# Kernel tuning notes

Hardware: AMD Instinct MI355X
Metric: run time of the kernel (lower is better)

The kernel has to match this reference:

```python
import jax, jax.numpy as jnp
import numpy as np
from jax import lax

B, L, D_MODEL = 2, 4096, 1024
D_INNER = 2 * D_MODEL          # expand=2
D_STATE = D_INNER              # required: complex einsum contracts d_inner vs d_state
DT_RANK = 64                   # ceil(1024/16)
D_CONV = 4


def setup_inputs() -> dict:
    key = jax.random.key(0)
    ks = jax.random.split(key, 16)
    s = lambda *sh: 1.0 / np.sqrt(sh[-1])
    return {
        "hidden_states": jax.random.normal(ks[0], (B, L, D_MODEL), jnp.float32),
        "delta": jax.random.normal(ks[1], (B, L, DT_RANK), jnp.float32),
        # in_proj: Linear(d_model -> 2*d_inner), no bias
        "in_proj_w": jax.random.normal(ks[2], (2 * D_INNER, D_MODEL), jnp.float32) * s(D_MODEL),
        # depthwise causal conv1d: (out=d_inner, in/groups=1, k)
        "conv_w": jax.random.normal(ks[3], (D_INNER, 1, D_CONV), jnp.float32) * s(D_CONV),
        "conv_b": jax.random.normal(ks[4], (D_INNER,), jnp.float32) * 0.01,
        # ComplexStateSpace: only A_real affects the real output (x is real)
        "A_real": jax.random.normal(ks[5], (D_STATE, D_STATE), jnp.float32) * 0.1 / np.sqrt(D_STATE),
        # MIMO linears (torch Linear weight layout [out, in])
        "B_w": jax.random.normal(ks[6], (D_STATE, D_INNER), jnp.float32) * 0.1 * s(D_INNER),
        "C_w": jax.random.normal(ks[7], (D_INNER, D_STATE), jnp.float32) * 0.1 * s(D_STATE),
        "D_w": jax.random.normal(ks[8], (D_INNER, D_INNER), jnp.float32) * 0.1 * s(D_INNER),
        # SelectiveScan params
        "dt_proj_w": jax.random.normal(ks[9], (D_INNER, DT_RANK), jnp.float32) * 0.01,
        "dt_proj_b": jax.random.normal(ks[10], (D_INNER,), jnp.float32) * 0.01,
        "A_log": jax.random.uniform(ks[11], (D_INNER,), jnp.float32, -4.0, -1.0),
        "D_ss": jnp.ones((D_INNER,), jnp.float32),
        # out_proj: Linear(d_inner -> d_model), no bias
        "out_proj_w": jax.random.normal(ks[12], (D_MODEL, D_INNER), jnp.float32) * s(D_INNER),
    }


def reference(hidden_states, delta, in_proj_w, conv_w, conv_b, A_real,
              B_w, C_w, D_w, dt_proj_w, dt_proj_b, A_log, D_ss, out_proj_w):
    d_inner = A_log.shape[0]
    # in_proj + split
    xz = jnp.einsum('bld,ed->ble', hidden_states, in_proj_w)
    x, z = xz[..., :d_inner], xz[..., d_inner:]
    # depthwise causal conv1d (left-pad k-1 == torch pad both + truncate to L)
    xc = jnp.swapaxes(x, 1, 2)                      # [b, d, l]
    xc = lax.conv_general_dilated(xc, conv_w, window_strides=(1,),
                                  padding=[(D_CONV - 1, 0)],
                                  feature_group_count=d_inner)
    x = jnp.swapaxes(xc, 1, 2) + conv_b             # [b, l, d]
    x = jax.nn.silu(x)
    # ComplexStateSpace: real part of (x @ (A_real + iA_imag)) == x @ A_real
    x = x + jnp.einsum('bls,st->blt', x, A_real)
    # MIMO SSM: state_t = cumsum(B x)_t ; y_t = C state_t + D x_t  (vectorized)
    Bx = jnp.einsum('bld,sd->bls', x, B_w)          # [b, l, d_state]
    states = jnp.cumsum(Bx, axis=1)
    x_mimo = jnp.einsum('bls,es->ble', states, C_w) + jnp.einsum('bld,ed->ble', x, D_w)
    x = x + x_mimo
    # SelectiveScan: state = state * exp(dlt * A) + u, A = -exp(A_log)
    dlt = jax.nn.softplus(jnp.einsum('blr,dr->bld', delta, dt_proj_w) + dt_proj_b)
    decay = jnp.exp(dlt * (-jnp.exp(A_log)))        # [b, l, d], in (0, 1)

    def step(state, inp):
        dec, u = inp
        state = state * dec + u
        return state, state

    init = jnp.zeros_like(x[:, 0])
    _, scan_states = lax.scan(step, init,
                              (jnp.swapaxes(decay, 0, 1), jnp.swapaxes(x, 0, 1)))
    x = jnp.swapaxes(scan_states, 0, 1) + x * D_ss
    # gate + out projection
    out = x * jax.nn.silu(z)
    return jnp.einsum('ble,de->bld', out, out_proj_w)
```

## Files before the change

### kernel.cpp

```cpp
#include <hip/hip_runtime.h>
#include <cstdint>
#include <cstddef>


typedef unsigned short u16;
typedef __bf16 bf16x8 __attribute__((ext_vector_type(8)));
typedef float  f32x4  __attribute__((ext_vector_type(4)));

#define BDIM 256
#define M_ROWS 8192
#define LSEQ   4096
#define DI     2048
#define NCH    64
#define CLEN   64

__device__ __forceinline__ float bf2f(u16 h) {
    return __uint_as_float(((unsigned int)h) << 16);
}
__device__ __forceinline__ u16 f2bf(float f) {
    unsigned int u = __float_as_uint(f);
    u = u + 0x7fffu + ((u >> 16) & 1u);
    return (u16)(u >> 16);
}
__device__ __forceinline__ float siluf(float v) { return v / (1.0f + __expf(-v)); }

__device__ __forceinline__ void load16_to_lds(const u16* g, u16* l) {
    __builtin_amdgcn_global_load_lds((const __attribute__((address_space(1))) void*)g,
                                     (__attribute__((address_space(3))) void*)l,
                                     16, 0, 0);
}

__global__ void k_cvt_all(const float* __restrict__ hs, const float* __restrict__ inproj,
                          const float* __restrict__ Bw, const float* __restrict__ Cw,
                          const float* __restrict__ outw, const float* __restrict__ delta,
                          const float* __restrict__ dtw, const float* __restrict__ Areal,
                          const float* __restrict__ Dw, const float* __restrict__ Alog,
                          u16* __restrict__ XH, u16* __restrict__ W1, u16* __restrict__ WBb,
                          u16* __restrict__ WC, u16* __restrict__ WO, u16* __restrict__ DLT,
                          u16* __restrict__ WDT, u16* __restrict__ Pb, u16* __restrict__ Db,
                          float* __restrict__ NA) {
    long i = (long)(blockIdx.x * BDIM + threadIdx.x) * 4;
    if (i >= 32112640L) {
        long j = i - 32112640L;
        if (j < 2048) {
            float4 v = *reinterpret_cast<const float4*>(Alog + j);
            float4 o = {-__expf(v.x), -__expf(v.y), -__expf(v.z), -__expf(v.w)};
            *reinterpret_cast<float4*>(NA + j) = o;
        }
        return;
    }
    const float* src; u16* dst; long off; bool diag = false;
    if      (i <  8388608L) { src = hs;     dst = XH;  off = 0L; }
    else if (i < 12582912L) { src = inproj; dst = W1;  off = 8388608L; }
    else if (i < 16777216L) { src = Bw;     dst = WBb; off = 12582912L; }
    else if (i < 20971520L) { src = Cw;     dst = WC;  off = 16777216L; }
    else if (i < 23068672L) { src = outw;   dst = WO;  off = 20971520L; }
    else if (i < 23592960L) { src = delta;  dst = DLT; off = 23068672L; }
    else if (i < 23724032L) { src = dtw;    dst = WDT; off = 23592960L; }
    else if (i < 27918336L) { src = Areal;  dst = Pb;  off = 23724032L; diag = true; }
    else                    { src = Dw;     dst = Db;  off = 27918336L; diag = true; }
    long j = i - off;
    float4 v = *reinterpret_cast<const float4*>(src + j);
    if (diag) {
        int r = (int)(j >> 11), c = (int)(j & 2047);
        if (r >= c && r < c + 4) (&v.x)[r - c] += 1.0f;
    }
    ushort2 a = {f2bf(v.x), f2bf(v.y)};
    ushort2 b = {f2bf(v.z), f2bf(v.w)};
    *reinterpret_cast<ushort2*>(dst + j)     = a;
    *reinterpret_cast<ushort2*>(dst + j + 2) = b;
}

__device__ __forceinline__ void gemm_core(
    u16* As, u16* Bs,
    const u16* __restrict__ A1, const u16* __restrict__ W1, int K1,
    const u16* __restrict__ A2, const u16* __restrict__ W2, int K2,
    int N, float* __restrict__ outf, u16* __restrict__ outb, u16* __restrict__ outb2,
    const float* __restrict__ bias1, const float* __restrict__ bias2,
    int m0, int n0, int mode) {
    const int tid  = threadIdx.x;
    const int wave = tid >> 6;
    const int lane = tid & 63;
    const int wm = (wave >> 1) * 64;
    const int wn = (wave & 1) * 64;
    const int lr = lane & 15;
    const int lq = lane >> 4;
    const int stg_row = lane >> 3;
    const int stg_col = (((lane & 7) ^ (lane >> 3)) << 3);

    f32x4 acc[4][4] = {};

    const int nt1 = K1 >> 6;
    const int nt2 = K2 >> 6;
    const int ntot = nt1 + nt2;

    for (int kt = 0; kt < ntot; ++kt) {
        const u16* Ap; const u16* Wp; int ld, k0;
        if (kt < nt1) { Ap = A1; Wp = W1; ld = K1; k0 = kt << 6; }
        else          { Ap = A2; Wp = W2; ld = K2; k0 = (kt - nt1) << 6; }
        #pragma unroll
        for (int i = 0; i < 4; ++i) {
            int chunk = wave * 4 + i;
            int r = chunk * 8 + stg_row;
            load16_to_lds(Ap + (size_t)(m0 + r) * ld + (k0 + stg_col), As + chunk * 512);
            load16_to_lds(Wp + (size_t)(n0 + r) * ld + (k0 + stg_col), Bs + chunk * 512);
        }
        __syncthreads();
        #pragma unroll
        for (int kk = 0; kk < 64; kk += 32) {
            bf16x8 af[4], bfr[4];
            #pragma unroll
            for (int i = 0; i < 4; ++i) {
                int R = wm + i * 16 + lr;
                af[i] = *reinterpret_cast<const bf16x8*>(
                    &As[R * 64 + ((kk + lq * 8) ^ ((R & 7) << 3))]);
            }
            #pragma unroll
            for (int i = 0; i < 4; ++i) {
                int R = wn + i * 16 + lr;
                bfr[i] = *reinterpret_cast<const bf16x8*>(
                    &Bs[R * 64 + ((kk + lq * 8) ^ ((R & 7) << 3))]);
            }
            #pragma unroll
            for (int mi = 0; mi < 4; ++mi)
                #pragma unroll
                for (int ni = 0; ni < 4; ++ni)
                    acc[mi][ni] = __builtin_amdgcn_mfma_f32_16x16x32_bf16(
                        af[mi], bfr[ni], acc[mi][ni], 0, 0, 0);
        }
        __syncthreads();
    }

    if (mode == 8) {
        #pragma unroll
        for (int mi = 0; mi < 4; ++mi) {
            #pragma unroll
            for (int ni = 0; ni < 4; ++ni) {
                int row = m0 + wm + mi * 16 + lq * 4;
                int col = n0 + wn + ni * 16 + lr;
                ushort4 v;
                v.x = f2bf(acc[mi][ni][0]); v.y = f2bf(acc[mi][ni][1]);
                v.z = f2bf(acc[mi][ni][2]); v.w = f2bf(acc[mi][ni][3]);
                *reinterpret_cast<ushort4*>(outb + (size_t)col * 2048 + row) = v;
            }
        }
        return;
    }

    #pragma unroll
    for (int mi = 0; mi < 4; ++mi) {
        #pragma unroll
        for (int ni = 0; ni < 4; ++ni) {
            #pragma unroll
            for (int j = 0; j < 4; ++j) {
                int row = m0 + wm + mi * 16 + lq * 4 + j;
                int col = n0 + wn + ni * 16 + lr;
                float v = acc[mi][ni][j];
                if (mode == 6) {
                    if (col < 2048) outb [(size_t)row * 2048 + col]        = f2bf(v);
                    else            outb2[(size_t)row * 2048 + col - 2048] = f2bf(v);
                } else if (mode == 5) {
                    float dlt = v + bias1[col];
                    float sp  = (dlt > 15.f) ? dlt : __logf(1.f + __expf(dlt));
                    outb[(size_t)row * N + col] = f2bf(bias2[col] * sp);
                } else if (mode == 2) {
                    outf[(size_t)row * N + col] = v;
                } else {
                    outb[(size_t)row * N + col] = f2bf(v);
                }
            }
        }
    }
}

__device__ __forceinline__ void tile_coords(int q, int T, int gn, int& m0, int& n0) {
    int nloc = T >> 3;
    int nid  = (q & 7) * nloc + (q >> 3);
    m0 = (nid / gn) * 128;
    n0 = (nid % gn) * 128;
}

__global__ __launch_bounds__(256, 4)
void k_batch1(const u16* __restrict__ XH, const u16* __restrict__ W1,
              const u16* __restrict__ WBb, const u16* __restrict__ Pb,
              const u16* __restrict__ Db,
              u16* __restrict__ PBt, u16* __restrict__ WXp,
              u16* __restrict__ XB, u16* __restrict__ ZB) {
    __shared__ u16 As[128 * 64];
    __shared__ u16 Bs[128 * 64];
    int bid = blockIdx.x;
    int m0, n0;
    if (bid < 256) {
        tile_coords(bid, 256, 16, m0, n0);
        gemm_core(As, Bs, Pb, WBb, DI, nullptr, nullptr, 0, DI,
                  nullptr, PBt, nullptr, nullptr, nullptr, m0, n0, 0);
    } else if (bid < 512) {
        tile_coords(bid - 256, 256, 16, m0, n0);
        gemm_core(As, Bs, Db, Pb, DI, nullptr, nullptr, 0, DI,
                  nullptr, WXp, nullptr, nullptr, nullptr, m0, n0, 0);
    } else {
        tile_coords(bid - 512, 2048, 32, m0, n0);
        gemm_core(As, Bs, XH, W1, 1024, nullptr, nullptr, 0, 4096,
                  nullptr, XB, ZB, nullptr, nullptr, m0, n0, 6);
    }
}

__global__ __launch_bounds__(256, 4)
void k_conv_pre3(const u16* __restrict__ x, const float* __restrict__ w,
                 const float* __restrict__ b, u16* __restrict__ out,
                 const u16* __restrict__ PBt, const u16* __restrict__ WC,
                 u16* __restrict__ WCBp) {
    __shared__ u16 As[128 * 64];
    __shared__ u16 Bs[128 * 64];
    if (blockIdx.x < 256) {
        int m0, n0;
        tile_coords(blockIdx.x, 256, 16, m0, n0);
        gemm_core(As, Bs, PBt, WC, DI, nullptr, nullptr, 0, DI,
                  nullptr, WCBp, nullptr, nullptr, nullptr, m0, n0, 8);
        return;
    }
    int idx = (blockIdx.x - 256) * BDIM + threadIdx.x;
    int d  = idx & (DI - 1);
    int bl = idx >> 11;
    int l  = bl & (LSEQ - 1);
    float4 wv = *reinterpret_cast<const float4*>(w + d * 4);
    float wj[4] = {wv.x, wv.y, wv.z, wv.w};
    float acc = b[d];
    #pragma unroll
    for (int j = 0; j < 4; ++j) {
        int ll = l - 3 + j;
        if (ll >= 0) acc += wj[j] * bf2f(x[(size_t)(bl - 3 + j) * DI + d]);
    }
    out[idx] = f2bf(siluf(acc));
}

__global__ __launch_bounds__(256, 4)
void k_batch2(const u16* __restrict__ XC, const u16* __restrict__ WCBp,
              const u16* __restrict__ DLT, const u16* __restrict__ WDT,
              const float* __restrict__ dtb, const float* __restrict__ NA,
              u16* __restrict__ BXC, u16* __restrict__ LD) {
    __shared__ u16 As[128 * 64];
    __shared__ u16 Bs[128 * 64];
    int bid  = blockIdx.x;
    int half = bid >> 1;
    int m0, n0;
    tile_coords(half, 1024, 16, m0, n0);
    if ((bid & 1) == 0) {
        gemm_core(As, Bs, XC, WCBp, DI, nullptr, nullptr, 0, DI,
                  nullptr, BXC, nullptr, nullptr, nullptr, m0, n0, 0);
    } else {
        gemm_core(As, Bs, DLT, WDT, 64, nullptr, nullptr, 0, DI,
                  nullptr, LD, nullptr, dtb, NA, m0, n0, 5);
    }
}

template <int MODE>
__global__ __launch_bounds__(256, 4)
void k_gemm(const u16* __restrict__ A1, const u16* __restrict__ W1, int K1,
            const u16* __restrict__ A2, const u16* __restrict__ W2, int K2,
            int N, float* __restrict__ outf, u16* __restrict__ outb) {
    __shared__ u16 As[128 * 64];
    __shared__ u16 Bs[128 * 64];
    int bid = blockIdx.x + gridDim.x * blockIdx.y;
    int m0, n0;
    tile_coords(bid, gridDim.x * gridDim.y, gridDim.x, m0, n0);
    gemm_core(As, Bs, A1, W1, K1, A2, W2, K2, N,
              outf, outb, nullptr, nullptr, nullptr, m0, n0, MODE);
}

__global__ void k_cumsum_p1(const u16* __restrict__ Bx, float* __restrict__ aux) {
    int t = blockIdx.x * BDIM + threadIdx.x;
    int s = t & (DI - 1);
    int c = (t >> 11) & (NCH - 1);
    int b = t >> 17;
    const u16* p = Bx + ((size_t)(b * LSEQ + c * CLEN) * DI) + s;
    float sum = 0.f;
    for (int i = 0; i < CLEN; ++i) sum += bf2f(p[(size_t)i * DI]);
    aux[t] = sum;
}
__global__ void k_cumsum_p23(const u16* __restrict__ Bx, const float* __restrict__ aux,
                             u16* x3) {
    int t = blockIdx.x * BDIM + threadIdx.x;
    int s = t & (DI - 1);
    int c = (t >> 11) & (NCH - 1);
    int b = t >> 17;
    float run = 0.f;
    for (int j = 0; j < c; ++j) run += aux[(b * NCH + j) * DI + s];
    size_t base = ((size_t)(b * LSEQ + c * CLEN) * DI) + s;
    for (int i = 0; i < CLEN; ++i) {
        size_t ix = base + (size_t)i * DI;
        run += bf2f(Bx[ix]);
        x3[ix] = f2bf(run + bf2f(x3[ix]));
    }
}

__global__ void k_scan_p1(const u16* __restrict__ ld_, const u16* __restrict__ u,
                          float* __restrict__ auxA, float* __restrict__ auxS) {
    int t = blockIdx.x * BDIM + threadIdx.x;
    int d = t & (DI - 1);
    int c = (t >> 11) & (NCH - 1);
    int b = t >> 17;
    size_t base = ((size_t)(b * LSEQ + c * CLEN) * DI) + d;
    float ap = 1.f, s = 0.f;
    for (int i = 0; i < CLEN; ++i) {
        size_t ix = base + (size_t)i * DI;
        float a = __expf(bf2f(ld_[ix]));
        s = fmaf(a, s, bf2f(u[ix]));
        ap *= a;
    }
    auxA[t] = ap; auxS[t] = s;
}
__global__ void k_scan_p23(const u16* __restrict__ ld_, const u16* __restrict__ u,
                           const float* __restrict__ auxA, const float* __restrict__ auxS,
                           const u16* __restrict__ z, const float* __restrict__ Dss,
                           u16* __restrict__ outb) {
    int t = blockIdx.x * BDIM + threadIdx.x;
    int d = t & (DI - 1);
    int c = (t >> 11) & (NCH - 1);
    int b = t >> 17;
    float s = 0.f;
    for (int j = 0; j < c; ++j) {
        int i = (b * NCH + j) * DI + d;
        s = fmaf(auxA[i], s, auxS[i]);
    }
    size_t base = ((size_t)(b * LSEQ + c * CLEN) * DI) + d;
    float dss = Dss[d];
    for (int i = 0; i < CLEN; ++i) {
        size_t ix = base + (size_t)i * DI;
        float a = __expf(bf2f(ld_[ix]));
        float uu = bf2f(u[ix]);
        s = fmaf(a, s, uu);
        float x4 = s + uu * dss;
        float zz = bf2f(z[ix]);
        outb[ix] = f2bf(x4 * siluf(zz));
    }
}

extern "C" void kernel_launch(void* const* d_in, const int* in_sizes, int n_in,
                              void* d_out, int out_size, void* d_ws, size_t ws_size,
                              hipStream_t stream) {
    const float* hs     = (const float*)d_in[0];
    const float* delta  = (const float*)d_in[1];
    const float* inproj = (const float*)d_in[2];
    const float* convw  = (const float*)d_in[3];
    const float* convb  = (const float*)d_in[4];
    const float* Areal  = (const float*)d_in[5];
    const float* Bw     = (const float*)d_in[6];
    const float* Cw     = (const float*)d_in[7];
    const float* Dw     = (const float*)d_in[8];
    const float* dtw    = (const float*)d_in[9];
    const float* dtb    = (const float*)d_in[10];
    const float* Alog   = (const float*)d_in[11];
    const float* Dss    = (const float*)d_in[12];
    const float* outw   = (const float*)d_in[13];
    float* out = (float*)d_out;

    const size_t SZ_ACT = (size_t)M_ROWS * DI * 2;
    char* p = (char*)d_ws;
    u16* ZB  = (u16*)p; p += SZ_ACT;
    u16* XB  = (u16*)p;
    u16* X3  = XB;      p += SZ_ACT;
    u16* XC  = (u16*)p;
    u16* OUT = XC;      p += SZ_ACT;
    u16* BXC = (u16*)p; p += SZ_ACT;
    u16* WCBp= (u16*)p; p += SZ_ACT;
    u16* XH  = (u16*)p;
    u16* LD  = XH;
                        p += (size_t)M_ROWS * 1024 * 2;
    u16* W1  = (u16*)p; p += (size_t)4096 * 1024 * 2;
    u16* WBb = (u16*)p; p += (size_t)DI * DI * 2;
    u16* WC  = (u16*)p; p += (size_t)DI * DI * 2;
    u16* Pb  = (u16*)p; p += (size_t)DI * DI * 2;
    u16* Db  = (u16*)p; p += (size_t)DI * DI * 2;
    u16* PBt = (u16*)p; p += (size_t)DI * DI * 2;
    u16* WXp = (u16*)p; p += (size_t)DI * DI * 2;
    u16* WO  = (u16*)p; p += (size_t)1024 * DI * 2;
    u16* WDT = (u16*)p; p += (size_t)DI * 64 * 2;
    u16* DLT = (u16*)p; p += (size_t)M_ROWS * 64 * 2;
    float* aux1 = (float*)p; p += (size_t)2 * NCH * DI * 4;
    float* auxA = (float*)p; p += (size_t)2 * NCH * DI * 4;
    float* auxS = (float*)p; p += (size_t)2 * NCH * DI * 4;
    float* NA   = (float*)p; p += (size_t)DI * 4;

    k_cvt_all<<<31362, BDIM, 0, stream>>>(hs, inproj, Bw, Cw, outw, delta, dtw,
                                          Areal, Dw, Alog,
                                          XH, W1, WBb, WC, WO, DLT, WDT, Pb, Db, NA);
    k_batch1<<<2560, BDIM, 0, stream>>>(XH, W1, WBb, Pb, Db, PBt, WXp, XB, ZB);
    k_conv_pre3<<<256 + (M_ROWS * DI) / BDIM, BDIM, 0, stream>>>(
        XB, convw, convb, XC, PBt, WC, WCBp);
    k_batch2<<<2048, BDIM, 0, stream>>>(XC, WCBp, DLT, WDT, dtb, NA, BXC, LD);
    k_cumsum_p1<<<(2 * NCH * DI) / BDIM, BDIM, 0, stream>>>(BXC, aux1);
    k_gemm<0><<<dim3(16, 64), BDIM, 0, stream>>>(XC, WXp, DI, nullptr, nullptr, 0,
                                                 DI, nullptr, X3);
    k_cumsum_p23<<<(2 * NCH * DI) / BDIM, BDIM, 0, stream>>>(BXC, aux1, X3);
    k_scan_p1<<<(2 * NCH * DI) / BDIM, BDIM, 0, stream>>>(LD, X3, auxA, auxS);
    k_scan_p23<<<(2 * NCH * DI) / BDIM, BDIM, 0, stream>>>(LD, X3, auxA, auxS,
                                                           ZB, Dss, OUT);
    k_gemm<2><<<dim3(8, 64), BDIM, 0, stream>>>(OUT, WO, DI, nullptr, nullptr, 0,
                                                1024, out, nullptr);
}
```

Measured before the change: 693.1 us.

## Merge XC GEMMs into one wide-N launch and remap tiles per XCD column

The two GEMMs that read XC (against WCB and WX) are combined into one N=4096 GEMM by placing WXp right after WCBp, so one launch writes both BXC and X3 through the split-output mode. The delta projection GEMM is interleaved in the same grid. tile_coords now gives each XCD a contiguous band of N columns and walks M inside it, which is meant to improve L2 reuse of weight tiles. This saves one kernel launch and lets the XC A-tiles be shared within a launch, but it changes the block scheduling pattern for every GEMM.

```diff
diff --git a/kernel.cpp b/kernel.cpp
--- a/kernel.cpp
+++ b/kernel.cpp
@@ -173,11 +173,13 @@
     }
 }
 
-__device__ __forceinline__ void tile_coords(int q, int T, int gn, int& m0, int& n0) {
-    int nloc = T >> 3;
-    int nid  = (q & 7) * nloc + (q >> 3);
-    m0 = (nid / gn) * 128;
-    n0 = (nid % gn) * 128;
+__device__ __forceinline__ void tile_coords(int q, int gm, int gn, int& m0, int& n0) {
+    int xcd = q & 7;
+    int loc = q >> 3;
+    int cl  = loc / gm;
+    int r   = loc - cl * gm;
+    m0 = r * 128;
+    n0 = (xcd * (gn >> 3) + cl) * 128;
 }
 
 __global__ __launch_bounds__(256, 4)
@@ -191,15 +193,15 @@
     int bid = blockIdx.x;
     int m0, n0;
     if (bid < 256) {
-        tile_coords(bid, 256, 16, m0, n0);
+        tile_coords(bid, 16, 16, m0, n0);
         gemm_core(As, Bs, Pb, WBb, DI, nullptr, nullptr, 0, DI,
                   nullptr, PBt, nullptr, nullptr, nullptr, m0, n0, 0);
     } else if (bid < 512) {
-        tile_coords(bid - 256, 256, 16, m0, n0);
+        tile_coords(bid - 256, 16, 16, m0, n0);
         gemm_core(As, Bs, Db, Pb, DI, nullptr, nullptr, 0, DI,
                   nullptr, WXp, nullptr, nullptr, nullptr, m0, n0, 0);
     } else {
-        tile_coords(bid - 512, 2048, 32, m0, n0);
+        tile_coords(bid - 512, 64, 32, m0, n0);
         gemm_core(As, Bs, XH, W1, 1024, nullptr, nullptr, 0, 4096,
                   nullptr, XB, ZB, nullptr, nullptr, m0, n0, 6);
     }
@@ -214,7 +216,7 @@
     __shared__ u16 Bs[128 * 64];
     if (blockIdx.x < 256) {
         int m0, n0;
-        tile_coords(blockIdx.x, 256, 16, m0, n0);
+        tile_coords(blockIdx.x, 16, 16, m0, n0);
         gemm_core(As, Bs, PBt, WC, DI, nullptr, nullptr, 0, DI,
                   nullptr, WCBp, nullptr, nullptr, nullptr, m0, n0, 8);
         return;
@@ -235,20 +237,25 @@
 }
 
 __global__ __launch_bounds__(256, 4)
-void k_batch2(const u16* __restrict__ XC, const u16* __restrict__ WCBp,
-              const u16* __restrict__ DLT, const u16* __restrict__ WDT,
-              const float* __restrict__ dtb, const float* __restrict__ NA,
-              u16* __restrict__ BXC, u16* __restrict__ LD) {
+void k_batch36(const u16* __restrict__ XC, const u16* __restrict__ WCB2,
+               const u16* __restrict__ DLT, const u16* __restrict__ WDT,
+               const float* __restrict__ dtb, const float* __restrict__ NA,
+               u16* __restrict__ BXC, u16* __restrict__ X3, u16* __restrict__ LD) {
     __shared__ u16 As[128 * 64];
     __shared__ u16 Bs[128 * 64];
-    int bid  = blockIdx.x;
-    int half = bid >> 1;
+    int bid = blockIdx.x;
+    int g   = bid >> 3;
+    int l8  = bid & 7;
+    int t3  = g % 3;
     int m0, n0;
-    tile_coords(half, 1024, 16, m0, n0);
-    if ((bid & 1) == 0) {
-        gemm_core(As, Bs, XC, WCBp, DI, nullptr, nullptr, 0, DI,
-                  nullptr, BXC, nullptr, nullptr, nullptr, m0, n0, 0);
+    if (t3 < 2) {
+        int q = ((g / 3) * 2 + t3) * 8 + l8;
+        tile_coords(q, 64, 32, m0, n0);
+        gemm_core(As, Bs, XC, WCB2, DI, nullptr, nullptr, 0, 4096,
+                  nullptr, BXC, X3, nullptr, nullptr, m0, n0, 6);
     } else {
+        int q = (g / 3) * 8 + l8;
+        tile_coords(q, 64, 16, m0, n0);
         gemm_core(As, Bs, DLT, WDT, 64, nullptr, nullptr, 0, DI,
                   nullptr, LD, nullptr, dtb, NA, m0, n0, 5);
     }
@@ -263,7 +270,7 @@
     __shared__ u16 Bs[128 * 64];
     int bid = blockIdx.x + gridDim.x * blockIdx.y;
     int m0, n0;
-    tile_coords(bid, gridDim.x * gridDim.y, gridDim.x, m0, n0);
+    tile_coords(bid, gridDim.y, gridDim.x, m0, n0);
     gemm_core(As, Bs, A1, W1, K1, A2, W2, K2, N,
               outf, outb, nullptr, nullptr, nullptr, m0, n0, MODE);
 }
@@ -363,7 +370,9 @@
     u16* XC  = (u16*)p;
     u16* OUT = XC;      p += SZ_ACT;
     u16* BXC = (u16*)p; p += SZ_ACT;
-    u16* WCBp= (u16*)p; p += SZ_ACT;
+    u16* WCBp= (u16*)p;
+    u16* WXp = WCBp + (size_t)DI * DI;
+                        p += SZ_ACT;
     u16* XH  = (u16*)p;
     u16* LD  = XH;
                         p += (size_t)M_ROWS * 1024 * 2;
@@ -373,7 +382,7 @@
     u16* Pb  = (u16*)p; p += (size_t)DI * DI * 2;
     u16* Db  = (u16*)p; p += (size_t)DI * DI * 2;
     u16* PBt = (u16*)p; p += (size_t)DI * DI * 2;
-    u16* WXp = (u16*)p; p += (size_t)DI * DI * 2;
+    p += (size_t)DI * DI * 2;
     u16* WO  = (u16*)p; p += (size_t)1024 * DI * 2;
     u16* WDT = (u16*)p; p += (size_t)DI * 64 * 2;
     u16* DLT = (u16*)p; p += (size_t)M_ROWS * 64 * 2;
@@ -388,10 +397,8 @@
     k_batch1<<<2560, BDIM, 0, stream>>>(XH, W1, WBb, Pb, Db, PBt, WXp, XB, ZB);
     k_conv_pre3<<<256 + (M_ROWS * DI) / BDIM, BDIM, 0, stream>>>(
         XB, convw, convb, XC, PBt, WC, WCBp);
-    k_batch2<<<2048, BDIM, 0, stream>>>(XC, WCBp, DLT, WDT, dtb, NA, BXC, LD);
+    k_batch36<<<3072, BDIM, 0, stream>>>(XC, WCBp, DLT, WDT, dtb, NA, BXC, X3, LD);
     k_cumsum_p1<<<(2 * NCH * DI) / BDIM, BDIM, 0, stream>>>(BXC, aux1);
-    k_gemm<0><<<dim3(16, 64), BDIM, 0, stream>>>(XC, WXp, DI, nullptr, nullptr, 0,
-                                                 DI, nullptr, X3);
     k_cumsum_p23<<<(2 * NCH * DI) / BDIM, BDIM, 0, stream>>>(BXC, aux1, X3);
     k_scan_p1<<<(2 * NCH * DI) / BDIM, BDIM, 0, stream>>>(LD, X3, auxA, auxS);
     k_scan_p23<<<(2 * NCH * DI) / BDIM, BDIM, 0, stream>>>(LD, X3, auxA, auxS,
```

After: 700.1 us. No clear change (+1.0%).
